# Performance work log

Hardware: AMD Instinct MI355X
Metric: run time of the kernel (lower is better)

## Reference

```python
import jax, jax.numpy as jnp
import numpy as np
import math

B, N, H, NH, L, NC = 8, 128, 128, 4, 4, 1
DH = H // NH
EPS = 1e-5

def _gelu(x):
    return jax.nn.gelu(x, approximate=False)  # torch nn.GELU default is exact erf

def _ln(x, g, b):
    m = x.mean(-1, keepdims=True)
    v = ((x - m) ** 2).mean(-1, keepdims=True)
    return (x - m) / jnp.sqrt(v + EPS) * g + b

def _bn(x, mask, g, b):
    # BatchNorm1d over valid (unpadded) nodes only, batch statistics (train mode)
    m = mask[..., None].astype(x.dtype)
    cnt = m.sum()
    mu = (x * m).sum((0, 1)) / cnt
    var = (((x - mu) ** 2) * m).sum((0, 1)) / cnt
    return (x - mu) / jnp.sqrt(var + EPS) * g + b

def _forward(e, u, atom_emb, bond_emb, eigw_W, eigw_b, mha_norm_g, mha_norm_b, qkv_W, qkv_b, out_W, out_b, ffn_norm_g, ffn_norm_b, ffn1_W, ffn1_b, ffn2_W, ffn2_b, dec_W, dec_b, fe1_W, fe1_b, fe2_W, fe2_b, pre_W, pre_b, f1_W, f1_b, bn1_g, bn1_b, f2_W, f2_b, bn2_g, bn2_b, lin_W, lin_b, node_feat, edge_feat, length):
    Bx, Nx = e.shape
    node_mask = jnp.arange(Nx)[None, :] < length[:, None]                        # [B,N]
    edge_mask = (node_mask[:, :, None] & node_mask[:, None, :]).astype(e.dtype)  # [B,src,dst]
    # SineEncoding
    div = jnp.exp(jnp.arange(0, H, 2, dtype=e.dtype) * (-math.log(10000.0) / H))
    pe = (e * 100.0)[:, :, None] * div
    eeig = jnp.concatenate([e[..., None], jnp.sin(pe), jnp.cos(pe)], axis=-1)    # [B,N,H+1]
    eig = eeig @ eigw_W.T + eigw_b                                               # [B,N,H]
    # multi-head self-attention over eigenvalue tokens with key padding mask
    xm = _ln(eig, mha_norm_g, mha_norm_b)
    qkv = xm @ qkv_W.T + qkv_b
    q, k, v = jnp.split(qkv, 3, axis=-1)
    q = q.reshape(Bx, Nx, NH, DH).transpose(0, 2, 1, 3)
    k = k.reshape(Bx, Nx, NH, DH).transpose(0, 2, 1, 3)
    v = v.reshape(Bx, Nx, NH, DH).transpose(0, 2, 1, 3)
    scores = jnp.einsum('bhqd,bhkd->bhqk', q, k) / math.sqrt(DH)
    scores = jnp.where(node_mask[:, None, None, :], scores, -jnp.inf)
    attn = jax.nn.softmax(scores, axis=-1)                                       # [B,NH,N,N]
    ctx = jnp.einsum('bhqk,bhkd->bhqd', attn, v).transpose(0, 2, 1, 3).reshape(Bx, Nx, H)
    eig = eig + (ctx @ out_W.T + out_b)
    y = _ln(eig, ffn_norm_g, ffn_norm_b)
    y = _gelu(y @ ffn1_W.T + ffn1_b) @ ffn2_W.T + ffn2_b
    eig = eig + y
    new_e = (eig @ dec_W.T + dec_b).transpose(0, 2, 1)                           # [B,NH,N]
    # spectral bases: identity + u @ diag(new_e_k) @ u^T per head, as fused diagonal scale
    filters = jnp.einsum('bnm,bkm,bpm->bnpk', u, new_e, u)                       # [B,N,N,NH]
    eye = jnp.broadcast_to(jnp.eye(Nx, dtype=e.dtype)[None, :, :, None], (Bx, Nx, Nx, 1))
    bases = jnp.concatenate([eye, filters], axis=-1)                             # [B,N,N,NH+1]
    bases = _gelu(_gelu(bases @ fe1_W.T + fe1_b) @ fe2_W.T + fe2_b)              # [B,N,N,H]
    xf = atom_emb[node_feat]                                                     # [B,N,H]
    ea = bond_emb[edge_feat]                                                     # [B,N,N,H]
    for l in range(L):
        # copy_u gather + per-edge FFN * bases + masked scatter-sum to dst
        msg = _gelu((xf[:, :, None, :] + ea) @ pre_W[l].T + pre_b[l]) * bases
        aggr = jnp.einsum('bijh,bij->bjh', msg, edge_mask)
        xf = xf + aggr
        y = xf @ f1_W[l].T + f1_b[l]
        y = jax.nn.relu(_bn(y, node_mask, bn1_g[l], bn1_b[l]))
        y = y @ f2_W[l].T + f2_b[l]
        y = jax.nn.relu(_bn(y, node_mask, bn2_g[l], bn2_b[l]))
        xf = xf + y
    nm = node_mask[..., None].astype(e.dtype)
    h = (xf * nm).sum(1) / length[:, None].astype(e.dtype)                       # AvgPooling over valid nodes
    h = h @ lin_W.T + lin_b
    return h, new_e, attn

def setup_inputs():
    key = jax.random.key(0)
    ks = iter(jax.random.split(key, 64))
    def w(*shape):
        return jax.random.normal(next(ks), shape, dtype=jnp.float32) * 0.02
    z = lambda *s: jnp.zeros(s, dtype=jnp.float32)
    o = lambda *s: jnp.ones(s, dtype=jnp.float32)
    e = jax.random.uniform(next(ks), (B, N), dtype=jnp.float32) * 2.0
    u = jnp.linalg.qr(jax.random.normal(next(ks), (B, N, N), dtype=jnp.float32))[0]
    inp = {
        'e': e, 'u': u,
        'atom_emb': w(40, H), 'bond_emb': w(10, H).at[0].set(0.0),
        'eigw_W': w(H, H + 1), 'eigw_b': z(H),
        'mha_norm_g': o(H), 'mha_norm_b': z(H),
        'qkv_W': w(3 * H, H), 'qkv_b': z(3 * H),
        'out_W': w(H, H), 'out_b': z(H),
        'ffn_norm_g': o(H), 'ffn_norm_b': z(H),
        'ffn1_W': w(H, H), 'ffn1_b': z(H),
        'ffn2_W': w(H, H), 'ffn2_b': z(H),
        'dec_W': w(NH, H), 'dec_b': z(NH),
        'fe1_W': w(H, NH + 1), 'fe1_b': z(H),
        'fe2_W': w(H, H), 'fe2_b': z(H),
        'pre_W': w(L, H, H), 'pre_b': z(L, H),
        'f1_W': w(L, H, H), 'f1_b': z(L, H),
        'bn1_g': o(L, H), 'bn1_b': z(L, H),
        'f2_W': w(L, H, H), 'f2_b': z(L, H),
        'bn2_g': o(L, H), 'bn2_b': z(L, H),
        'lin_W': w(NC, H), 'lin_b': z(NC),
        'node_feat': jax.random.randint(next(ks), (B, N), 0, 40),
        'edge_feat': jax.random.randint(next(ks), (B, N, N), 0, 10),
        'length': 64 + jax.random.randint(next(ks), (B,), 0, N - 63),
    }
    return inp

def reference(e, u, atom_emb, bond_emb, eigw_W, eigw_b, mha_norm_g, mha_norm_b, qkv_W, qkv_b, out_W, out_b, ffn_norm_g, ffn_norm_b, ffn1_W, ffn1_b, ffn2_W, ffn2_b, dec_W, dec_b, fe1_W, fe1_b, fe2_W, fe2_b, pre_W, pre_b, f1_W, f1_b, bn1_g, bn1_b, f2_W, f2_b, bn2_g, bn2_b, lin_W, lin_b, node_feat, edge_feat, length):
    return _forward(e, u, atom_emb, bond_emb, eigw_W, eigw_b, mha_norm_g, mha_norm_b, qkv_W, qkv_b, out_W, out_b, ffn_norm_g, ffn_norm_b, ffn1_W, ffn1_b, ffn2_W, ffn2_b, dec_W, dec_b, fe1_W, fe1_b, fe2_W, fe2_b, pre_W, pre_b, f1_W, f1_b, bn1_g, bn1_b, f2_W, f2_b, bn2_g, bn2_b, lin_W, lin_b, node_feat, edge_feat, length)
```

## Files before the change

### kernel.cpp

```cpp
#include <hip/hip_runtime.h>
#include <hip/hip_bf16.h>
#include <math.h>

#define BB 8
#define NN 128
#define HH 128
#define NHD 4
#define DHD 32
#define LAY 4
#define EPSV 1e-5f

typedef __hip_bfloat16 bf16;
typedef unsigned short ushortt;
typedef short bf16x8 __attribute__((ext_vector_type(8)));
typedef float f32x4 __attribute__((ext_vector_type(4)));

__device__ __forceinline__ float b2f(bf16 x){ return __bfloat162float(x); }
__device__ __forceinline__ bf16 f2b(float x){ return __float2bfloat16(x); }
__device__ __forceinline__ float us2f(ushortt u){ return __uint_as_float(((unsigned)u)<<16); }
__device__ __forceinline__ ushortt f2us(float x){ bf16 b=__float2bfloat16(x); return *(ushortt*)&b; }
__device__ __forceinline__ float gelu_f(float x){ return 0.5f*x*(1.0f+erff(x*0.7071067811865476f)); }
__device__ __forceinline__ float gelu_h(float x){
  float t = 0.7978845608028654f*x*(1.0f + 0.044715f*x*x);
  float e = __expf(2.0f*t);
  float th = 1.0f - 2.0f/(e + 1.0f);
  return 0.5f*x*(1.0f + th);
}
__device__ __forceinline__ float erf_fast(float x){
  float ax = fabsf(x);
  float t = __builtin_amdgcn_rcpf(__builtin_fmaf(0.3275911f, ax, 1.0f));
  float p = __builtin_fmaf(1.061405429f, t, -1.453152027f);
  p = __builtin_fmaf(p, t, 1.421413741f);
  p = __builtin_fmaf(p, t, -0.284496736f);
  p = __builtin_fmaf(p, t, 0.254829592f);
  p = p*t;
  float e = __expf(-ax*ax);
  float y = __builtin_fmaf(-p, e, 1.0f);
  return __builtin_copysignf(y, x);
}
__device__ __forceinline__ float gelu_fe(float x){
  return 0.5f*x*(1.0f + erf_fast(x*0.7071067811865476f));
}


__global__ __launch_bounds__(256) void k_front(
    const float* __restrict__ fe2W, const float* __restrict__ preW,
    const float* __restrict__ outW, const float* __restrict__ ffn1W,
    const float* __restrict__ ffn2W, const float* __restrict__ f1W,
    const float* __restrict__ f2W, const float* __restrict__ aemb,
    const int* __restrict__ nf, const float* __restrict__ bemb,
    const float* __restrict__ preb,
    ushortt* __restrict__ wbf, float* __restrict__ gs, float* __restrict__ xf0,
    float* __restrict__ outWT, float* __restrict__ ffn1WT, float* __restrict__ ffn2WT,
    float* __restrict__ f1WT, float* __restrict__ f2WT, float* __restrict__ bondWall,
    const float* __restrict__ e, const float* __restrict__ eigW,
    const float* __restrict__ eigb, const float* __restrict__ g,
    const float* __restrict__ bt, const float* __restrict__ qkvW,
    const float* __restrict__ qkvb,
    float* __restrict__ eigout, float* __restrict__ q,
    float* __restrict__ kT, float* __restrict__ v){
  int blk = blockIdx.x;
  int tid = threadIdx.x;
  if (blk < 512){
    int idx = blk*256 + tid;
    if (idx < 10240) gs[idx] = 0.f;
    if (idx < 81920){
      float vv = (idx < 16384) ? fe2W[idx] : preW[idx - 16384];
      wbf[idx] = f2us(vv);
    }
    if (idx < 131072){
      int node = idx >> 7, h2 = idx & 127;
      xf0[idx] = aemb[nf[node]*HH + h2];
    }
    if (idx < 16384){ int o = idx>>7, m = idx&127;
      outWT[m*128+o]  = outW[idx];
      ffn1WT[m*128+o] = ffn1W[idx];
      ffn2WT[m*128+o] = ffn2W[idx];
    }
    if (idx < 65536){ int l = idx>>14, r = idx&16383; int o = r>>7, m = r&127;
      f1WT[l*16384 + m*128+o] = f1W[idx];
      f2WT[l*16384 + m*128+o] = f2W[idx];
    }
    if (idx < 5120){
      int l = idx / 1280; int r = idx - l*1280; int e2 = r >> 7; int hcol = r & 127;
      const float* br = bemb + e2*128;
      const float* wr = preW + l*16384 + hcol*128;
      float acc = preb[l*128 + hcol];
      for (int m=0;m<128;m++) acc += br[m]*wr[m];
      bondWall[idx] = acc;
    }
    return;
  }
  int sub = tid >> 7, lt = tid & 127;
  int row = (blk - 512)*2 + sub;
  int b = row >> 7, n = row & 127;
  __shared__ float ee[2][129]; __shared__ float buf[2][128]; __shared__ float xm[2][128];
  float ev = e[row];
  if (lt < 64){
    float dv = expf(-0.1439115683121279f * (float)lt);
    float pe = ev * 100.0f * dv;
    ee[sub][1+lt] = sinf(pe);
    ee[sub][65+lt] = cosf(pe);
  }
  if (lt == 0) ee[sub][0] = ev;
  __syncthreads();
  float x = eigb[lt];
  {
    const float* er = eigW + lt*129;
    for (int k2=0;k2<129;k2++) x += ee[sub][k2]*er[k2];
  }
  eigout[row*HH+lt] = x;
  buf[sub][lt]=x; __syncthreads();
  for (int s2=64;s2>0;s2>>=1){ if(lt<s2) buf[sub][lt]+=buf[sub][lt+s2]; __syncthreads(); }
  float mean = buf[sub][0]*(1.0f/128.0f); __syncthreads();
  float d = x-mean; buf[sub][lt]=d*d; __syncthreads();
  for (int s2=64;s2>0;s2>>=1){ if(lt<s2) buf[sub][lt]+=buf[sub][lt+s2]; __syncthreads(); }
  float var = buf[sub][0]*(1.0f/128.0f);
  xm[sub][lt] = d*rsqrtf(var+EPSV)*g[lt]+bt[lt];
  __syncthreads();
  #pragma unroll
  for (int s3=0;s3<3;s3++){
    float acc = qkvb[s3*HH+lt];
    const float* wt = qkvW + (s3*HH + lt)*128;
    for (int m=0;m<HH;m++) acc += xm[sub][m]*wt[m];
    if (s3==0) q[row*HH+lt]=acc;
    else if (s3==1) kT[b*16384 + lt*128 + n]=acc;
    else v[row*HH+lt]=acc;
  }
}

__global__ __launch_bounds__(512) void k_attc(const float* __restrict__ q,
    const float* __restrict__ kT, const float* __restrict__ v,
    const float* __restrict__ eig, const int* __restrict__ length,
    const float* __restrict__ outWT, const float* __restrict__ outb,
    const float* __restrict__ fng, const float* __restrict__ fnb,
    const float* __restrict__ w1T, const float* __restrict__ b1,
    const float* __restrict__ w2T, const float* __restrict__ b2,
    const float* __restrict__ dW, const float* __restrict__ db,
    float* __restrict__ newe, float* __restrict__ outp){
  int row = blockIdx.x; int b = row>>7, qi = row&127;
  int tid = threadIdx.x;
  int hg = tid>>7, lt = tid&127;
  int len = length[b];
  __shared__ float qv[4][DHD];
  __shared__ float red[4][128];
  __shared__ float satt[4][128];
  __shared__ float part[4][128];
  __shared__ float sc[128], sbuf[128], sxm[128], stt[128], sx[128];
  if (lt < DHD) qv[hg][lt] = q[(b*NN+qi)*HH + hg*DHD + lt];
  __syncthreads();
  float s = -1e30f;
  if (lt < len){
    const float* kr = kT + b*16384 + hg*DHD*128 + lt;
    float scr=0.f;
    for (int d2=0; d2<DHD; d2++) scr += qv[hg][d2]*kr[d2*128];
    s = scr * 0.17677669529663687f;
  }
  red[hg][lt]=s; __syncthreads();
  for (int st=64;st>0;st>>=1){ if(lt<st) red[hg][lt]=fmaxf(red[hg][lt],red[hg][lt+st]); __syncthreads(); }
  float mx = red[hg][0]; __syncthreads();
  float pp = (lt<len)? expf(s-mx):0.0f;
  red[hg][lt]=pp; __syncthreads();
  for (int st=64;st>0;st>>=1){ if(lt<st) red[hg][lt]+=red[hg][lt+st]; __syncthreads(); }
  float a = pp / red[hg][0];
  satt[hg][lt] = a;
  outp[4104 + ((b*NHD+hg)*NN+qi)*NN + lt] = a;
  __syncthreads();
  {
    int hd = lt>>5;
    float p=0.f;
    for (int j=hg*32; j<hg*32+32; j++) p += satt[hd][j]*v[(b*NN+j)*HH+lt];
    part[hg][lt]=p;
  }
  __syncthreads();
  if (tid < 128) sc[tid] = (part[0][tid]+part[1][tid])+(part[2][tid]+part[3][tid]);
  __syncthreads();
  {
    float p = (hg==0)? outb[lt] : 0.f;
    for (int m=hg*32; m<hg*32+32; m++) p += sc[m]*outWT[m*128+lt];
    part[hg][lt]=p;
  }
  __syncthreads();
  if (tid < 128){
    float x = eig[row*HH+tid] + ((part[0][tid]+part[1][tid])+(part[2][tid]+part[3][tid]));
    sx[tid] = x; sbuf[tid] = x;
  }
  __syncthreads();
  for (int s2=64;s2>0;s2>>=1){ if(tid<s2) sbuf[tid]+=sbuf[tid+s2]; __syncthreads(); }
  float mean = sbuf[0]*(1.f/128.f); __syncthreads();
  if (tid < 128){ float d = sx[tid]-mean; sbuf[tid]=d*d; }
  __syncthreads();
  for (int s2=64;s2>0;s2>>=1){ if(tid<s2) sbuf[tid]+=sbuf[tid+s2]; __syncthreads(); }
  float var = sbuf[0]*(1.f/128.f);
  if (tid < 128){
    float d = sx[tid]-mean;
    sxm[tid] = d*rsqrtf(var+EPSV)*fng[tid]+fnb[tid];
  }
  __syncthreads();
  {
    float p = (hg==0)? b1[lt] : 0.f;
    for (int m=hg*32; m<hg*32+32; m++) p += sxm[m]*w1T[m*128+lt];
    part[hg][lt]=p;
  }
  __syncthreads();
  if (tid < 128) stt[tid]=gelu_f((part[0][tid]+part[1][tid])+(part[2][tid]+part[3][tid]));
  __syncthreads();
  {
    float p = (hg==0)? b2[lt] : 0.f;
    for (int m=hg*32; m<hg*32+32; m++) p += stt[m]*w2T[m*128+lt];
    part[hg][lt]=p;
  }
  __syncthreads();
  if (tid < 128) sx[tid] = sx[tid] + ((part[0][tid]+part[1][tid])+(part[2][tid]+part[3][tid]));
  __syncthreads();
  if (tid < 4){
    float acc = db[tid];
    const float* wr = dW + tid*HH;
    for (int h2=0;h2<HH;h2++) acc += sx[h2]*wr[h2];
    int idx=(b*NHD+tid)*NN+qi;
    newe[idx]=acc; outp[8+idx]=acc;
  }
}

__global__ __launch_bounds__(256) void k_bx(const float* __restrict__ u,
    const float* __restrict__ newe,
    const float* __restrict__ w1g, const float* __restrict__ b1g,
    const ushortt* __restrict__ w2bf, const float* __restrict__ b2g,
    const int* __restrict__ length,
    bf16* __restrict__ bases,
    const float* __restrict__ xf0, const ushortt* __restrict__ wbfl0,
    float* __restrict__ xfW){
  int blk = blockIdx.x;
  int tid = threadIdx.x;
  int lane = tid & 63, w = tid >> 6, quad = lane >> 4, l15 = lane & 15;
  __shared__ alignas(16) char us[38400];
  if (blk >= 2048){
    int blk2 = blk - 2048;
    int b = blk2 >> 2, rq = blk2 & 3;
    ushortt* sA = (ushortt*)us;
    for (int idx = tid; idx < 1024; idx += 256){
      int r = idx >> 5, c = idx & 31;
      int gr = b*128 + rq*32 + r;
      float4 xv = ((const float4*)xf0)[gr*32 + c];
      ushort4 o;
      o.x=f2us(xv.x); o.y=f2us(xv.y); o.z=f2us(xv.z); o.w=f2us(xv.w);
      *(ushort4*)&sA[r*136 + c*4] = o;
    }
    __syncthreads();
    f32x4 acc[2][2];
    #pragma unroll
    for (int mt=0;mt<2;mt++)
      #pragma unroll
      for (int nt=0;nt<2;nt++) acc[mt][nt] = (f32x4){0.f,0.f,0.f,0.f};
    #pragma unroll
    for (int kk = 0; kk < 128; kk += 32){
      bf16x8 af[2], bfr[2];
      #pragma unroll
      for (int mt=0;mt<2;mt++) af[mt] = *(const bf16x8*)&sA[(mt*16+l15)*136 + kk + quad*8];
      #pragma unroll
      for (int nt=0;nt<2;nt++) bfr[nt] = *(const bf16x8*)&wbfl0[((w*2+nt)*16+l15)*128 + kk + quad*8];
      #pragma unroll
      for (int mt=0;mt<2;mt++)
        #pragma unroll
        for (int nt=0;nt<2;nt++)
          acc[mt][nt] = __builtin_amdgcn_mfma_f32_16x16x32_bf16(af[mt], bfr[nt], acc[mt][nt], 0, 0, 0);
    }
    #pragma unroll
    for (int mt=0;mt<2;mt++)
      #pragma unroll
      for (int nt=0;nt<2;nt++){
        int h = (w*2+nt)*16 + l15;
        #pragma unroll
        for (int reg=0;reg<4;reg++){
          int prr = rq*32 + mt*16 + quad*4 + reg;
          xfW[(b*128 + prr)*128 + h] = acc[mt][nt][reg];
        }
      }
    return;
  }
  int bi = blk >> 1;
  int r0 = (blk & 1)*64;
  int b = bi >> 7;
  int nloc = bi & 127;
  int len = length[b];
  if (nloc >= len || r0 >= len) return;
  int pr = r0 + w*16 + l15;
  ushortt* sW2 = (ushortt*)us;
  float* w1a = (float*)(us + 32768);
  float* w1b = (float*)(us + 34816);
  float* b2s = (float*)(us + 35840);
  float* cn  = (float*)(us + 36352);
  for (int idx = tid; idx < 2048; idx += 256){
    int r = idx >> 4, cb = idx & 15;
    *(uint4*)&sW2[r*128 + ((cb*8) ^ ((r&15)<<3))] = *(const uint4*)&w2bf[r*128 + cb*8];
  }
  if (tid < 128){
    w1a[tid*4+0] = b1g[tid];
    w1a[tid*4+1] = w1g[tid*5+0];
    w1a[tid*4+2] = w1g[tid*5+1];
    w1a[tid*4+3] = w1g[tid*5+2];
    w1b[tid*2+0] = w1g[tid*5+3];
    w1b[tid*2+1] = w1g[tid*5+4];
    b2s[tid] = b2g[tid];
  }
  for (int idx = tid; idx < 512; idx += 256){
    int k = idx >> 7, m = idx & 127;
    cn[k*128+m] = u[(b*NN+nloc)*NN + m] * newe[(b*NHD+k)*NN + m];
  }
  __syncthreads();
  bool wact = (r0 + w*16) < len;
  f32x4 acc[8];
  #pragma unroll
  for (int nt=0;nt<8;nt++) acc[nt] = (f32x4){0.f,0.f,0.f,0.f};
  if (wact){
    float f0=0.f, f1=0.f, f2v=0.f, f3=0.f;
    const float4* ur = (const float4*)(u + ((size_t)b*NN + pr)*NN);
    for (int m4 = quad*8; m4 < quad*8+8; m4++){
      float4 uv = ur[m4];
      int m = m4*4;
      f0 += cn[m]*uv.x; f0 += cn[m+1]*uv.y; f0 += cn[m+2]*uv.z; f0 += cn[m+3]*uv.w;
      f1 += cn[128+m]*uv.x; f1 += cn[128+m+1]*uv.y; f1 += cn[128+m+2]*uv.z; f1 += cn[128+m+3]*uv.w;
      f2v += cn[256+m]*uv.x; f2v += cn[256+m+1]*uv.y; f2v += cn[256+m+2]*uv.z; f2v += cn[256+m+3]*uv.w;
      f3 += cn[384+m]*uv.x; f3 += cn[384+m+1]*uv.y; f3 += cn[384+m+2]*uv.z; f3 += cn[384+m+3]*uv.w;
    }
    f0 += __shfl_xor(f0, 16, 64);  f0 += __shfl_xor(f0, 32, 64);
    f1 += __shfl_xor(f1, 16, 64);  f1 += __shfl_xor(f1, 32, 64);
    f2v += __shfl_xor(f2v, 16, 64); f2v += __shfl_xor(f2v, 32, 64);
    f3 += __shfl_xor(f3, 16, 64);  f3 += __shfl_xor(f3, 32, 64);
    float dg = (pr == nloc) ? 1.0f : 0.0f;
    for (int kk = 0; kk < 128; kk += 32){
      bf16x8 af;
      #pragma unroll
      for (int j=0;j<8;j++){
        int m = kk + quad*8 + j;
        const float4 wa = *(const float4*)&w1a[m*4];
        const float2 wb = *(const float2*)&w1b[m*2];
        float a = wa.x + wa.y*dg + wa.z*f0 + wa.w*f1 + wb.x*f2v + wb.y*f3;
        af[j] = (short)f2us(gelu_fe(a));
      }
      #pragma unroll
      for (int nt=0;nt<8;nt++){
        int rowb = nt*16 + l15;
        int off = (kk + quad*8) ^ (l15 << 3);
        bf16x8 bfr = *(const bf16x8*)&sW2[rowb*128 + off];
        acc[nt] = __builtin_amdgcn_mfma_f32_16x16x32_bf16(af, bfr, acc[nt], 0, 0, 0);
      }
    }
  }
  __syncthreads();
  ushortt* sT = sW2;
  if (wact){
    #pragma unroll
    for (int nt=0;nt<8;nt++){
      int h = nt*16 + l15;
      float bb = b2s[h];
      #pragma unroll
      for (int reg=0;reg<4;reg++){
        int lr = w*16 + quad*4 + reg;
        sT[lr*132 + h] = f2us(gelu_fe(acc[nt][reg] + bb));
      }
    }
  }
  __syncthreads();
  int rmax = len - r0; if (rmax > 64) rmax = 64;
  ushort4* gout = (ushort4*)(bases + (size_t)bi*16384 + r0*128);
  for (int idx = tid; idx < rmax*32; idx += 256){
    int row = idx >> 5, seg = idx & 31;
    gout[idx] = *(const ushort4*)&sT[row*132 + seg*4];
  }
}


__global__ __launch_bounds__(256) void k_xwl2(const float* __restrict__ xfprev,
    const float* __restrict__ t2, const float* __restrict__ gsum2p,
    const float* __restrict__ gsq2p, const float* __restrict__ g2p,
    const float* __restrict__ bb2p, const int* __restrict__ length,
    const ushortt* __restrict__ wbfl, float* __restrict__ xfB,
    float* __restrict__ xfW){
  int blk = blockIdx.x;
  int b = blk >> 2, rq = blk & 3;
  int tid = threadIdx.x;
  int lane = tid & 63, w = tid >> 6, quad = lane >> 4, l15 = lane & 15;
  __shared__ alignas(16) ushortt sA[32*136];
  __shared__ float smu[128], sistd[128], sg[128], sbb[128];
  if (tid < 128){
    float cnt = 0.f;
    for (int q2=0;q2<BB;q2++) cnt += (float)length[q2];
    float mu = gsum2p[tid]/cnt;
    float var = gsq2p[tid]/cnt - mu*mu;
    smu[tid]=mu; sistd[tid]=rsqrtf(fmaxf(var,0.0f)+EPSV);
    sg[tid]=g2p[tid]; sbb[tid]=bb2p[tid];
  }
  __syncthreads();
  for (int idx = tid; idx < 1024; idx += 256){
    int r = idx >> 5, c = idx & 31;
    int gr = b*128 + rq*32 + r;
    float4 xv = ((const float4*)xfprev)[gr*32 + c];
    float4 tv = ((const float4*)t2)[gr*32 + c];
    int f0 = c*4;
    xv.x += fmaxf((tv.x-smu[f0+0])*sistd[f0+0]*sg[f0+0]+sbb[f0+0], 0.f);
    xv.y += fmaxf((tv.y-smu[f0+1])*sistd[f0+1]*sg[f0+1]+sbb[f0+1], 0.f);
    xv.z += fmaxf((tv.z-smu[f0+2])*sistd[f0+2]*sg[f0+2]+sbb[f0+2], 0.f);
    xv.w += fmaxf((tv.w-smu[f0+3])*sistd[f0+3]*sg[f0+3]+sbb[f0+3], 0.f);
    ((float4*)xfB)[gr*32 + c] = xv;
    ushort4 o;
    o.x=f2us(xv.x); o.y=f2us(xv.y); o.z=f2us(xv.z); o.w=f2us(xv.w);
    *(ushort4*)&sA[r*136 + c*4] = o;
  }
  __syncthreads();
  f32x4 acc[2][2];
  #pragma unroll
  for (int mt=0;mt<2;mt++)
    #pragma unroll
    for (int nt=0;nt<2;nt++) acc[mt][nt] = (f32x4){0.f,0.f,0.f,0.f};
  #pragma unroll
  for (int kk = 0; kk < 128; kk += 32){
    bf16x8 af[2], bfr[2];
    #pragma unroll
    for (int mt=0;mt<2;mt++) af[mt] = *(const bf16x8*)&sA[(mt*16+l15)*136 + kk + quad*8];
    #pragma unroll
    for (int nt=0;nt<2;nt++) bfr[nt] = *(const bf16x8*)&wbfl[((w*2+nt)*16+l15)*128 + kk + quad*8];
    #pragma unroll
    for (int mt=0;mt<2;mt++)
      #pragma unroll
      for (int nt=0;nt<2;nt++)
        acc[mt][nt] = __builtin_amdgcn_mfma_f32_16x16x32_bf16(af[mt], bfr[nt], acc[mt][nt], 0, 0, 0);
  }
  #pragma unroll
  for (int mt=0;mt<2;mt++)
    #pragma unroll
    for (int nt=0;nt<2;nt++){
      int h = (w*2+nt)*16 + l15;
      #pragma unroll
      for (int reg=0;reg<4;reg++){
        int prr = rq*32 + mt*16 + quad*4 + reg;
        xfW[(b*128 + prr)*128 + h] = acc[mt][nt][reg];
      }
    }
}

__global__ __launch_bounds__(512) void k_edge(const float* __restrict__ xfin, float* __restrict__ xfout,
    const bf16* __restrict__ bases, const float* __restrict__ xfW,
    const float* __restrict__ bondWl, const int* __restrict__ ef,
    const int* __restrict__ length,
    const float* __restrict__ w1t, const float* __restrict__ bias1,
    float* __restrict__ t1, float* __restrict__ gst){
  int bj = blockIdx.x; int b = bj >> 7, j = bj & 127;
  int len = length[b];
  int tid = threadIdx.x;
  int is = tid >> 6, hp = tid & 63;
  int h2 = hp*2;
  __shared__ float sBW[10][128];
  __shared__ int sEf[128];
  __shared__ float part[8][128];
  for (int idx = tid; idx < 1280; idx += 512) sBW[idx>>7][idx&127] = bondWl[idx];
  if (tid < 128) sEf[tid] = ef[(b*NN + tid)*NN + j];
  __syncthreads();
  float a0 = 0.f, a1 = 0.f;
  if (j < len){
    const float* xwb = xfW + b*NN*HH;
    const ushortt* bb = (const ushortt*)(bases + ((size_t)b*NN + j)*NN*HH);
    for (int i = is; i < len; i += 8){
      int ev = sEf[i];
      float2 xw = *(const float2*)&xwb[i*128 + h2];
      float2 bw = *(const float2*)&sBW[ev][h2];
      unsigned bv = *(const unsigned*)&bb[i*128 + h2];
      float v0 = gelu_h(xw.x + bw.x);
      float v1 = gelu_h(xw.y + bw.y);
      a0 += v0 * us2f((ushortt)(bv & 0xffffu));
      a1 += v1 * us2f((ushortt)(bv >> 16));
    }
  }
  part[is][h2] = a0; part[is][h2+1] = a1;
  __syncthreads();
  if (tid < 128){
    int o = (b*NN + j)*HH + tid;
    float xrow = xfin[o]
      + ((part[0][tid]+part[1][tid])+(part[2][tid]+part[3][tid]))
      + ((part[4][tid]+part[5][tid])+(part[6][tid]+part[7][tid]));
    xfout[o] = xrow;
    part[0][tid] = xrow;
  }
  __syncthreads();
  int h = tid & 127, ih = tid >> 7;
  float acc = (ih==0) ? bias1[h] : 0.f;
  {
    const float* wcol = w1t + h;
    int m0 = ih*32;
    for (int m = m0; m < m0+32; m++) acc += part[0][m]*wcol[m*128];
  }
  float* red = &sBW[0][0];
  __syncthreads();
  red[ih*128 + h] = acc; __syncthreads();
  if (tid < 128){
    float t1v = red[tid] + red[128+tid] + red[256+tid] + red[384+tid];
    t1[(b*NN + j)*HH + tid] = t1v;
    if (j < len){
      int bank = bj & 7;
      atomicAdd(&gst[bank*256 + tid], t1v);
      atomicAdd(&gst[bank*256 + 128 + tid], t1v*t1v);
    }
  }
}

__global__ __launch_bounds__(256) void k_g2s(const float* __restrict__ t1,
    const float* __restrict__ gstL,
    const float* __restrict__ g1, const float* __restrict__ bb1,
    const float* __restrict__ w2t, const float* __restrict__ bias2,
    const int* __restrict__ length, float* __restrict__ t2){
  int blk = blockIdx.x; int tid = threadIdx.x;
  int f = tid & 127, rh = tid >> 7;
  __shared__ float sy[4][128];
  __shared__ float red1[2][128], red2[2][128];
  int r0 = blk*4;
  float cnt = 0.f;
  for (int b=0;b<BB;b++) cnt += (float)length[b];
  float su = 0.f, sq = 0.f;
  #pragma unroll
  for (int k=0;k<8;k++){ su += gstL[k*256 + f]; sq += gstL[k*256 + 128 + f]; }
  float mu = su/cnt;
  float var = sq/cnt - mu*mu;
  float istd = rsqrtf(fmaxf(var,0.0f)+EPSV);
  float gg = g1[f], bbv = bb1[f];
  for (int idx = tid; idx < 512; idx += 256){
    int r = idx >> 7;
    float x = t1[(r0+r)*128 + f];
    float y = (x-mu)*istd*gg + bbv;
    sy[r][f] = fmaxf(y, 0.0f);
  }
  __syncthreads();
  float bsv = bias2[f];
  float s=0.f, s2=0.f;
  for (int rr = rh*2; rr < rh*2+2; rr++){
    int rg = r0 + rr; int b = rg >> 7, n = rg & 127;
    float acc = bsv;
    for (int m=0;m<128;m++) acc += sy[rr][m]*w2t[m*128+f];
    t2[rg*128+f] = acc;
    if (n < length[b]){ s += acc; s2 += acc*acc; }
  }
  red1[rh][f]=s; red2[rh][f]=s2; __syncthreads();
  if (tid < 128){
    atomicAdd((float*)&gstL[2048 + tid], red1[0][tid]+red1[1][tid]);
    atomicAdd((float*)&gstL[2048 + 128 + tid], red2[0][tid]+red2[1][tid]);
  }
}

__global__ void k_pool2(const float* __restrict__ xf, const float* __restrict__ t2,
                        const float* __restrict__ gsum2, const float* __restrict__ gsq2,
                        const float* __restrict__ g2, const float* __restrict__ bb2,
                        const int* __restrict__ length,
                        const float* lw, const float* lb, float* __restrict__ outp){
  int b = blockIdx.x, tid=threadIdx.x;
  int len = length[b];
  float cnt = 0.f;
  for (int q2=0;q2<BB;q2++) cnt += (float)length[q2];
  float mu = gsum2[tid]/cnt;
  float var = gsq2[tid]/cnt - mu*mu;
  float istd = rsqrtf(fmaxf(var,0.0f)+EPSV);
  float gg = g2[tid], bbv = bb2[tid];
  float s=0.f;
  for (int n2=0;n2<len;n2++){
    int o = (b*NN+n2)*HH+tid;
    float x = xf[o] + fmaxf((t2[o]-mu)*istd*gg+bbv, 0.0f);
    s += x;
  }
  s /= (float)len;
  __shared__ float red[128];
  red[tid]=s*lw[tid]; __syncthreads();
  for (int st=64;st>0;st>>=1){ if(tid<st) red[tid]+=red[tid+st]; __syncthreads(); }
  if (tid==0) outp[b]=red[0]+lb[0];
}


extern "C" void kernel_launch(void* const* d_in, const int* in_sizes, int n_in,
                              void* d_out, int out_size, void* d_ws, size_t ws_size,
                              hipStream_t stream) {
  (void)in_sizes; (void)n_in; (void)out_size; (void)ws_size;
  const float* e        = (const float*)d_in[0];
  const float* u        = (const float*)d_in[1];
  const float* atom_emb = (const float*)d_in[2];
  const float* bond_emb = (const float*)d_in[3];
  const float* eigw_W   = (const float*)d_in[4];
  const float* eigw_b   = (const float*)d_in[5];
  const float* mng      = (const float*)d_in[6];
  const float* mnb      = (const float*)d_in[7];
  const float* qkvW     = (const float*)d_in[8];
  const float* qkvb     = (const float*)d_in[9];
  const float* outW     = (const float*)d_in[10];
  const float* outb     = (const float*)d_in[11];
  const float* fng      = (const float*)d_in[12];
  const float* fnb      = (const float*)d_in[13];
  const float* ffn1W    = (const float*)d_in[14];
  const float* ffn1b    = (const float*)d_in[15];
  const float* ffn2W    = (const float*)d_in[16];
  const float* ffn2b    = (const float*)d_in[17];
  const float* decW     = (const float*)d_in[18];
  const float* decb     = (const float*)d_in[19];
  const float* fe1W     = (const float*)d_in[20];
  const float* fe1b     = (const float*)d_in[21];
  const float* fe2W     = (const float*)d_in[22];
  const float* fe2b     = (const float*)d_in[23];
  const float* preW     = (const float*)d_in[24];
  const float* preb     = (const float*)d_in[25];
  const float* f1W      = (const float*)d_in[26];
  const float* f1b      = (const float*)d_in[27];
  const float* bn1g     = (const float*)d_in[28];
  const float* bn1b     = (const float*)d_in[29];
  const float* f2W      = (const float*)d_in[30];
  const float* f2b      = (const float*)d_in[31];
  const float* bn2g     = (const float*)d_in[32];
  const float* bn2b     = (const float*)d_in[33];
  const float* linW     = (const float*)d_in[34];
  const float* linb     = (const float*)d_in[35];
  const int* nodef      = (const int*)d_in[36];
  const int* edgef      = (const int*)d_in[37];
  const int* length     = (const int*)d_in[38];

  float* outp = (float*)d_out;

  char* p = (char*)d_ws;
  auto alloc = [&](size_t bytes)->void*{ void* r=(void*)p; p += (bytes+255)&~(size_t)255; return r; };
  const int TOK = BB*NN*HH;
  float* eig   = (float*)alloc(TOK*4);
  float* q     = (float*)alloc(TOK*4);
  float* kT    = (float*)alloc(TOK*4);
  float* v     = (float*)alloc(TOK*4);
  float* newe  = (float*)alloc(BB*NHD*NN*4);
  bf16*  bases = (bf16*) alloc((size_t)BB*NN*NN*HH*2);
  float* xf0   = (float*)alloc(TOK*4);
  float* xfB   = (float*)alloc(TOK*4);
  float* xfC   = (float*)alloc(TOK*4);
  float* xfD   = (float*)alloc(TOK*4);
  float* t1    = (float*)alloc(TOK*4);
  float* t2    = (float*)alloc(TOK*4);
  float* xfW   = (float*)alloc(TOK*4);
  float* gs    = (float*)alloc(10240*4);
  ushortt* wbf = (ushortt*)alloc(81920*2);
  float* outWT = (float*)alloc(16384*4);
  float* ffn1WT= (float*)alloc(16384*4);
  float* ffn2WT= (float*)alloc(16384*4);
  float* f1WT  = (float*)alloc(65536*4);
  float* f2WT  = (float*)alloc(65536*4);
  float* bondWall = (float*)alloc(5120*4);

  k_front<<<1024, 256, 0, stream>>>(fe2W, preW, outW, ffn1W, ffn2W,
                                    f1W, f2W, atom_emb, nodef, bond_emb, preb,
                                    wbf, gs, xf0, outWT, ffn1WT, ffn2WT,
                                    f1WT, f2WT, bondWall,
                                    e, eigw_W, eigw_b, mng, mnb, qkvW, qkvb,
                                    eig, q, kT, v);

  k_attc<<<BB*NN, 512, 0, stream>>>(q, kT, v, eig, length,
                                    outWT, outb, fng, fnb,
                                    ffn1WT, ffn1b, ffn2WT, ffn2b,
                                    decW, decb, newe, outp);

  k_bx<<<2048 + BB*4, 256, 0, stream>>>(u, newe, fe1W, fe1b, wbf, fe2b, length,
                                        bases, xf0, wbf + 16384, xfW);

  const float* xfprev = xf0;
  float* xfcur = xfC;
  for (int l=0;l<LAY;l++){
    const ushortt* wbfl = wbf + 16384 + l*16384;
    float* gsl = gs + l*2560;
    float* gsp = gs + (l-1)*2560;
    if (l > 0){
      k_xwl2<<<BB*4, 256, 0, stream>>>(xfprev, t2, gsp+2048, gsp+2048+128,
                                       bn2g + (l-1)*HH, bn2b + (l-1)*HH,
                                       length, wbfl, xfB, xfW);
    }
    const float* xin = (l==0)? xf0 : xfB;
    k_edge<<<BB*NN, 512, 0, stream>>>(xin, xfcur, bases, xfW, bondWall + l*1280,
                                      edgef, length,
                                      f1WT + l*16384, f1b + l*HH, t1, gsl);
    k_g2s<<<256, 256, 0, stream>>>(t1, gsl, bn1g + l*HH, bn1b + l*HH,
                                   f2WT + l*16384, f2b + l*HH, length, t2);
    xfprev = xfcur;
    xfcur = (xfcur == xfC) ? xfD : xfC;
  }
  k_pool2<<<BB, 128, 0, stream>>>(xfprev, t2, gs+3*2560+2048, gs+3*2560+2048+128,
                                  bn2g + 3*HH, bn2b + 3*HH, length, linW, linb, outp);
}
```

Baseline: 388.8 us.

## Merge k_bx row-halves into one 512-thread block per node

k_bx previously launched two 256-thread blocks per (batch, node), each loading the full 32KB W2 tile into shared memory and computing cn. Now one 512-thread block covers all 128 rows, so the W2 staging and cn computation happen once per node. The output is written in two halves that reuse the shared staging buffer, with extra barriers between them. The xf0 GEMM side blocks are packed two per block. This adds syncs and lowers block-level parallelism.

```diff
diff --git a/kernel.cpp b/kernel.cpp
--- a/kernel.cpp
+++ b/kernel.cpp
@@ -222,7 +222,7 @@
   }
 }
 
-__global__ __launch_bounds__(256) void k_bx(const float* __restrict__ u,
+__global__ __launch_bounds__(512) void k_bx(const float* __restrict__ u,
     const float* __restrict__ newe,
     const float* __restrict__ w1g, const float* __restrict__ b1g,
     const ushortt* __restrict__ w2bf, const float* __restrict__ b2g,
@@ -232,13 +232,14 @@
     float* __restrict__ xfW){
   int blk = blockIdx.x;
   int tid = threadIdx.x;
-  int lane = tid & 63, w = tid >> 6, quad = lane >> 4, l15 = lane & 15;
   __shared__ alignas(16) char us[38400];
-  if (blk >= 2048){
-    int blk2 = blk - 2048;
-    int b = blk2 >> 2, rq = blk2 & 3;
-    ushortt* sA = (ushortt*)us;
-    for (int idx = tid; idx < 1024; idx += 256){
+  if (blk < 16){
+    int sub = tid >> 8, lt = tid & 255;
+    int item = blk*2 + sub;
+    int b = item >> 2, rq = item & 3;
+    int lane = lt & 63, w = lt >> 6, quad = lane >> 4, l15 = lane & 15;
+    ushortt* sA = (ushortt*)(us + sub*8704);
+    for (int idx = lt; idx < 1024; idx += 256){
       int r = idx >> 5, c = idx & 31;
       int gr = b*128 + rq*32 + r;
       float4 xv = ((const float4*)xf0)[gr*32 + c];
@@ -278,19 +279,19 @@
       }
     return;
   }
-  int bi = blk >> 1;
-  int r0 = (blk & 1)*64;
+  int bi = blk - 16;
   int b = bi >> 7;
   int nloc = bi & 127;
   int len = length[b];
-  if (nloc >= len || r0 >= len) return;
-  int pr = r0 + w*16 + l15;
+  if (nloc >= len) return;
+  int lane = tid & 63, w = tid >> 6, quad = lane >> 4, l15 = lane & 15;
+  int pr = w*16 + l15;
   ushortt* sW2 = (ushortt*)us;
   float* w1a = (float*)(us + 32768);
   float* w1b = (float*)(us + 34816);
   float* b2s = (float*)(us + 35840);
   float* cn  = (float*)(us + 36352);
-  for (int idx = tid; idx < 2048; idx += 256){
+  for (int idx = tid; idx < 2048; idx += 512){
     int r = idx >> 4, cb = idx & 15;
     *(uint4*)&sW2[r*128 + ((cb*8) ^ ((r&15)<<3))] = *(const uint4*)&w2bf[r*128 + cb*8];
   }
@@ -303,12 +304,12 @@
     w1b[tid*2+1] = w1g[tid*5+4];
     b2s[tid] = b2g[tid];
   }
-  for (int idx = tid; idx < 512; idx += 256){
-    int k = idx >> 7, m = idx & 127;
+  if (tid < 512){
+    int k = tid >> 7, m = tid & 127;
     cn[k*128+m] = u[(b*NN+nloc)*NN + m] * newe[(b*NHD+k)*NN + m];
   }
   __syncthreads();
-  bool wact = (r0 + w*16) < len;
+  bool wact = (w*16) < len;
   f32x4 acc[8];
   #pragma unroll
   for (int nt=0;nt<8;nt++) acc[nt] = (f32x4){0.f,0.f,0.f,0.f};
@@ -349,7 +350,7 @@
   }
   __syncthreads();
   ushortt* sT = sW2;
-  if (wact){
+  if (wact && w < 4){
     #pragma unroll
     for (int nt=0;nt<8;nt++){
       int h = nt*16 + l15;
@@ -362,11 +363,37 @@
     }
   }
   __syncthreads();
-  int rmax = len - r0; if (rmax > 64) rmax = 64;
-  ushort4* gout = (ushort4*)(bases + (size_t)bi*16384 + r0*128);
-  for (int idx = tid; idx < rmax*32; idx += 256){
-    int row = idx >> 5, seg = idx & 31;
-    gout[idx] = *(const ushort4*)&sT[row*132 + seg*4];
+  {
+    int rmax = len < 64 ? len : 64;
+    ushort4* gout = (ushort4*)(bases + (size_t)bi*16384);
+    for (int idx = tid; idx < rmax*32; idx += 512){
+      int row = idx >> 5, seg = idx & 31;
+      gout[idx] = *(const ushort4*)&sT[row*132 + seg*4];
+    }
+  }
+  __syncthreads();
+  if (wact && w >= 4){
+    #pragma unroll
+    for (int nt=0;nt<8;nt++){
+      int h = nt*16 + l15;
+      float bb = b2s[h];
+      #pragma unroll
+      for (int reg=0;reg<4;reg++){
+        int lr = (w-4)*16 + quad*4 + reg;
+        sT[lr*132 + h] = f2us(gelu_fe(acc[nt][reg] + bb));
+      }
+    }
+  }
+  __syncthreads();
+  {
+    int rmax2 = len - 64; if (rmax2 < 0) rmax2 = 0; if (rmax2 > 64) rmax2 = 64;
+    if (rmax2 > 0){
+      ushort4* gout = (ushort4*)(bases + (size_t)bi*16384 + 64*128);
+      for (int idx = tid; idx < rmax2*32; idx += 512){
+        int row = idx >> 5, seg = idx & 31;
+        gout[idx] = *(const ushort4*)&sT[row*132 + seg*4];
+      }
+    }
   }
 }
 
@@ -655,8 +682,8 @@
                                     ffn1WT, ffn1b, ffn2WT, ffn2b,
                                     decW, decb, newe, outp);
 
-  k_bx<<<2048 + BB*4, 256, 0, stream>>>(u, newe, fe1W, fe1b, wbf, fe2b, length,
-                                        bases, xf0, wbf + 16384, xfW);
+  k_bx<<<16 + BB*NN, 512, 0, stream>>>(u, newe, fe1W, fe1b, wbf, fe2b, length,
+                                       bases, xf0, wbf + 16384, xfW);
 
   const float* xfprev = xf0;
   float* xfcur = xfC;
```

New measurement: 382.2 us. Within noise of the previous version (-1.7%).
